# Kernel optimization log

Hardware: AMD Instinct MI355X
Metric: run time of the kernel (lower is better)

Reference implementation:

```python
import jax, jax.numpy as jnp
import numpy as np

B, S, E, Q = 4, 4096, 1024, 8  # batch, seq, embed_dim, n_qubits


def setup_inputs() -> dict:
    key = jax.random.key(0)
    k1, k2, k3 = jax.random.split(key, 3)
    x = jax.random.normal(k1, (B, S, E), dtype=jnp.float32)
    W_enc = jax.random.normal(k2, (Q, E), dtype=jnp.float32) * (1.0 / np.sqrt(E))
    W_dec = jax.random.normal(k3, (E, Q), dtype=jnp.float32) * (1.0 / np.sqrt(Q))
    return {"x": x, "W_enc": W_enc, "W_dec": W_dec}


def reference(x, W_enc, W_dec):
    # encode tokens to rotation angles: [B,S,Q]
    angles = jnp.einsum('bse,qe->bsq', x, W_enc)
    c = jnp.cos(angles)
    # Analytic state-vector result of the circuit:
    #   RX(theta_i) on |0> then CNOT chain + ring closure, measure <Z_i>.
    # Heisenberg picture gives:
    #   <Z_0> = prod_{j=1..Q-1} cos(theta_j)
    #   <Z_i> = prod_{j=0..i}   cos(theta_j)   (i >= 1)
    p = jnp.cumprod(c, axis=-1)                      # prefix products
    q0 = jnp.prod(c[..., 1:], axis=-1, keepdims=True)
    q = jnp.concatenate([q0, p[..., 1:]], axis=-1)   # [B,S,Q] expvals
    # decode back to embed_dim and add residual
    return jnp.einsum('bsq,eq->bse', q, W_dec) + x
```

## Files before the change

### kernel.cpp

```cpp
#include <hip/hip_runtime.h>


typedef float v2f __attribute__((ext_vector_type(2)));
typedef float v4f __attribute__((ext_vector_type(4)));

#define EDIM 1024
#define QDIM 8
#define NTOK 16384
#define BLOCK 256
#define G 4
#define ITERS 4
#define GRID (NTOK / (G * ITERS))

template<int CTRL>
__device__ __forceinline__ float dpp_add(float v) {
    int m = __builtin_amdgcn_update_dpp(0, __float_as_int(v), CTRL, 0xF, 0xF, true);
    return v + __int_as_float(m);
}

__device__ __forceinline__ float wave_sum63(float v) {
    v = dpp_add<0x111>(v);
    v = dpp_add<0x112>(v);
    v = dpp_add<0x114>(v);
    v = dpp_add<0x118>(v);
    v = dpp_add<0x142>(v);
    v = dpp_add<0x143>(v);
    return v;
}

template<int K>
__device__ __forceinline__ float scan_mul_step(float p, int laneq) {
    int m = __builtin_amdgcn_update_dpp(0, __float_as_int(p), 0x110 | K, 0xF, 0xF, true);
    float tmul = (laneq >= K) ? __int_as_float(m) : 1.0f;
    return p * tmul;
}

__global__ __launch_bounds__(BLOCK, 1)
void qattn_kernel(const float* __restrict__ x,
                  const float* __restrict__ W_enc,
                  const float* __restrict__ W_dec,
                  float* __restrict__ out)
{
    __shared__ float red[G][4][QDIM];
    __shared__ float qv_s[G][QDIM];

    const int t    = threadIdx.x;
    const int lane = t & 63;
    const int wave = t >> 6;
    const int e0   = t * 4;
    const int tok0 = blockIdx.x * (G * ITERS);

    v4f wenc[QDIM];
#pragma unroll
    for (int q = 0; q < QDIM; ++q)
        wenc[q] = *(const v4f*)(W_enc + q * EDIM + e0);
    v4f wdlo[4], wdhi[4];
#pragma unroll
    for (int j = 0; j < 4; ++j) {
        wdlo[j] = *(const v4f*)(W_dec + (e0 + j) * QDIM);
        wdhi[j] = *(const v4f*)(W_dec + (e0 + j) * QDIM + 4);
    }
#pragma unroll
    for (int q = 0; q < QDIM; ++q) asm volatile("" : "+v"(wenc[q]));
#pragma unroll
    for (int j = 0; j < 4; ++j) {
        asm volatile("" : "+v"(wdlo[j]));
        asm volatile("" : "+v"(wdhi[j]));
    }

    v4f xv[G];
#pragma unroll
    for (int i = 0; i < G; ++i)
        xv[i] = *(const v4f*)(x + (size_t)(tok0 + i) * EDIM + e0);

    for (int it = 0; it < ITERS; ++it) {
        v4f xn[G];
        if (it + 1 < ITERS) {
#pragma unroll
            for (int i = 0; i < G; ++i)
                xn[i] = *(const v4f*)(x + (size_t)(tok0 + (it + 1) * G + i) * EDIM + e0);
        }

        float ang[G][QDIM];
#pragma unroll
        for (int i = 0; i < G; ++i) {
            v2f x01 = (v2f){xv[i].x, xv[i].y};
            v2f x23 = (v2f){xv[i].z, xv[i].w};
#pragma unroll
            for (int q = 0; q < QDIM; ++q) {
                v2f acc = x01 * (v2f){wenc[q].x, wenc[q].y};
                acc = __builtin_elementwise_fma(x23, (v2f){wenc[q].z, wenc[q].w}, acc);
                ang[i][q] = acc.x + acc.y;
            }
        }
#pragma unroll
        for (int i = 0; i < G; ++i)
#pragma unroll
            for (int q = 0; q < QDIM; ++q)
                ang[i][q] = wave_sum63(ang[i][q]);

        if (lane == 63) {
#pragma unroll
            for (int i = 0; i < G; ++i) {
                *(v4f*)&red[i][wave][0] = (v4f){ang[i][0], ang[i][1], ang[i][2], ang[i][3]};
                *(v4f*)&red[i][wave][4] = (v4f){ang[i][4], ang[i][5], ang[i][6], ang[i][7]};
            }
        }
        __syncthreads();

        if (wave == 0 && lane < G * QDIM) {
            const int tk = lane >> 3;
            const int q  = lane & 7;
            float s = red[tk][0][q] + red[tk][1][q] + red[tk][2][q] + red[tk][3][q];
            float c = __cosf(s);

            float p = c;
            p = scan_mul_step<1>(p, q);
            p = scan_mul_step<2>(p, q);
            p = scan_mul_step<4>(p, q);

            float b = (q == 0) ? 1.0f : c;
            b = scan_mul_step<1>(b, q);
            b = scan_mul_step<2>(b, q);
            b = scan_mul_step<4>(b, q);

            if (q > 0)  qv_s[tk][q] = p;
            if (q == 7) qv_s[tk][0] = b;
        }
        __syncthreads();

#pragma unroll
        for (int i = 0; i < G; ++i) {
            v4f qlo = *(const v4f*)&qv_s[i][0];
            v4f qhi = *(const v4f*)&qv_s[i][4];
            float oacc[4];
#pragma unroll
            for (int j = 0; j < 4; ++j) {
                v4f a = qlo * wdlo[j];
                a = __builtin_elementwise_fma(qhi, wdhi[j], a);
                v2f hh = (v2f){a.x, a.y} + (v2f){a.z, a.w};
                oacc[j] = hh.x + hh.y;
            }
            v4f o = xv[i] + (v4f){oacc[0], oacc[1], oacc[2], oacc[3]};
            __builtin_nontemporal_store(o, (v4f*)(out + (size_t)(tok0 + it * G + i) * EDIM + e0));
        }

        if (it + 1 < ITERS) {
#pragma unroll
            for (int i = 0; i < G; ++i) xv[i] = xn[i];
        }
    }
}

extern "C" void kernel_launch(void* const* d_in, const int* in_sizes, int n_in,
                              void* d_out, int out_size, void* d_ws, size_t ws_size,
                              hipStream_t stream) {
    const float* x     = (const float*)d_in[0];
    const float* W_enc = (const float*)d_in[1];
    const float* W_dec = (const float*)d_in[2];
    float* out         = (float*)d_out;

    hipLaunchKernelGGL(qattn_kernel, dim3(GRID), dim3(BLOCK), 0, stream,
                       x, W_enc, W_dec, out);
}
```

Measured before the change: 31.40 us.

## Stage x tiles through LDS with async global_load_lds double buffering

Replaces the register prefetch of x with direct global-to-LDS async loads into a double-buffered shared tile, synchronised by manual vmcnt waits and raw barriers. It also splits the angle reduction into two halves to cut register pressure and raises launch bounds to allow up to four blocks per CU. The aim is better latency hiding and more occupancy for this bandwidth-bound kernel. The hand-written vmcnt counts are fragile: the nontemporal stores also increment vmcnt, so the waits may not order things correctly. The 32KB of LDS per block limits residency.

```diff
diff --git a/kernel.cpp b/kernel.cpp
--- a/kernel.cpp
+++ b/kernel.cpp
@@ -11,6 +11,11 @@
 #define G 4
 #define ITERS 4
 #define GRID (NTOK / (G * ITERS))
+
+#define GLOAD_LDS(gsrc, ldst)                                                  \
+    __builtin_amdgcn_global_load_lds(                                          \
+        (const __attribute__((address_space(1))) void*)(gsrc),                 \
+        (__attribute__((address_space(3))) void*)(ldst), 16, 0, 0)
 
 template<int CTRL>
 __device__ __forceinline__ float dpp_add(float v) {
@@ -35,12 +40,13 @@
     return p * tmul;
 }
 
-__global__ __launch_bounds__(BLOCK, 1)
+__global__ __launch_bounds__(BLOCK, 4)
 void qattn_kernel(const float* __restrict__ x,
                   const float* __restrict__ W_enc,
                   const float* __restrict__ W_dec,
                   float* __restrict__ out)
 {
+    __shared__ float xbuf[2][G][EDIM];
     __shared__ float red[G][4][QDIM];
     __shared__ float qv_s[G][QDIM];
 
@@ -60,53 +66,71 @@
         wdlo[j] = *(const v4f*)(W_dec + (e0 + j) * QDIM);
         wdhi[j] = *(const v4f*)(W_dec + (e0 + j) * QDIM + 4);
     }
+
 #pragma unroll
-    for (int q = 0; q < QDIM; ++q) asm volatile("" : "+v"(wenc[q]));
-#pragma unroll
-    for (int j = 0; j < 4; ++j) {
-        asm volatile("" : "+v"(wdlo[j]));
-        asm volatile("" : "+v"(wdhi[j]));
+    for (int i = 0; i < G; ++i) {
+        const float* src = x + (size_t)(tok0 + i) * EDIM + wave * 256 + lane * 4;
+        GLOAD_LDS(src, &xbuf[0][i][wave * 256]);
     }
 
-    v4f xv[G];
 #pragma unroll
-    for (int i = 0; i < G; ++i)
-        xv[i] = *(const v4f*)(x + (size_t)(tok0 + i) * EDIM + e0);
+    for (int it = 0; it < ITERS; ++it) {
+        const int cb = it & 1;
 
-    for (int it = 0; it < ITERS; ++it) {
-        v4f xn[G];
         if (it + 1 < ITERS) {
 #pragma unroll
-            for (int i = 0; i < G; ++i)
-                xn[i] = *(const v4f*)(x + (size_t)(tok0 + (it + 1) * G + i) * EDIM + e0);
+            for (int i = 0; i < G; ++i) {
+                const float* src = x + (size_t)(tok0 + (it + 1) * G + i) * EDIM
+                                   + wave * 256 + lane * 4;
+                GLOAD_LDS(src, &xbuf[cb ^ 1][i][wave * 256]);
+            }
         }
 
-        float ang[G][QDIM];
+        if (it == 0)                asm volatile("s_waitcnt vmcnt(4)" ::: "memory");
+        else if (it + 1 < ITERS)    asm volatile("s_waitcnt vmcnt(8)" ::: "memory");
+        else                        asm volatile("s_waitcnt vmcnt(4)" ::: "memory");
+        __builtin_amdgcn_sched_barrier(0);
+
+        v4f xv[G];
 #pragma unroll
-        for (int i = 0; i < G; ++i) {
-            v2f x01 = (v2f){xv[i].x, xv[i].y};
-            v2f x23 = (v2f){xv[i].z, xv[i].w};
+        for (int i = 0; i < G; ++i)
+            xv[i] = *(const v4f*)&xbuf[cb][i][e0];
+
 #pragma unroll
-            for (int q = 0; q < QDIM; ++q) {
-                v2f acc = x01 * (v2f){wenc[q].x, wenc[q].y};
-                acc = __builtin_elementwise_fma(x23, (v2f){wenc[q].z, wenc[q].w}, acc);
-                ang[i][q] = acc.x + acc.y;
+        for (int h = 0; h < 2; ++h) {
+            float ang[2][QDIM];
+#pragma unroll
+            for (int i = 0; i < 2; ++i) {
+                const int ii = h * 2 + i;
+                v2f x01 = (v2f){xv[ii].x, xv[ii].y};
+                v2f x23 = (v2f){xv[ii].z, xv[ii].w};
+#pragma unroll
+                for (int q = 0; q < QDIM; ++q) {
+                    v2f acc = x01 * (v2f){wenc[q].x, wenc[q].y};
+                    acc = __builtin_elementwise_fma(x23, (v2f){wenc[q].z, wenc[q].w}, acc);
+                    ang[i][q] = acc.x + acc.y;
+                }
+            }
+#pragma unroll
+            for (int i = 0; i < 2; ++i)
+#pragma unroll
+                for (int q = 0; q < QDIM; ++q)
+                    ang[i][q] = wave_sum63(ang[i][q]);
+
+            if (lane == 63) {
+#pragma unroll
+                for (int i = 0; i < 2; ++i) {
+                    *(v4f*)&red[h * 2 + i][wave][0] =
+                        (v4f){ang[i][0], ang[i][1], ang[i][2], ang[i][3]};
+                    *(v4f*)&red[h * 2 + i][wave][4] =
+                        (v4f){ang[i][4], ang[i][5], ang[i][6], ang[i][7]};
+                }
             }
         }
-#pragma unroll
-        for (int i = 0; i < G; ++i)
-#pragma unroll
-            for (int q = 0; q < QDIM; ++q)
-                ang[i][q] = wave_sum63(ang[i][q]);
 
-        if (lane == 63) {
-#pragma unroll
-            for (int i = 0; i < G; ++i) {
-                *(v4f*)&red[i][wave][0] = (v4f){ang[i][0], ang[i][1], ang[i][2], ang[i][3]};
-                *(v4f*)&red[i][wave][4] = (v4f){ang[i][4], ang[i][5], ang[i][6], ang[i][7]};
-            }
-        }
-        __syncthreads();
+        asm volatile("s_waitcnt lgkmcnt(0)" ::: "memory");
+        __builtin_amdgcn_s_barrier();
+        __builtin_amdgcn_sched_barrier(0);
 
         if (wave == 0 && lane < G * QDIM) {
             const int tk = lane >> 3;
@@ -127,7 +151,10 @@
             if (q > 0)  qv_s[tk][q] = p;
             if (q == 7) qv_s[tk][0] = b;
         }
-        __syncthreads();
+
+        asm volatile("s_waitcnt lgkmcnt(0)" ::: "memory");
+        __builtin_amdgcn_s_barrier();
+        __builtin_amdgcn_sched_barrier(0);
 
 #pragma unroll
         for (int i = 0; i < G; ++i) {
@@ -144,11 +171,6 @@
             v4f o = xv[i] + (v4f){oacc[0], oacc[1], oacc[2], oacc[3]};
             __builtin_nontemporal_store(o, (v4f*)(out + (size_t)(tok0 + it * G + i) * EDIM + e0));
         }
-
-        if (it + 1 < ITERS) {
-#pragma unroll
-            for (int i = 0; i < G; ++i) xv[i] = xn[i];
-        }
     }
 }
 
```

New measurement: 30.96 us. Within noise of the previous version (-1.4%).
